# Optimization experiments

Measured on AMD Instinct MI355X. Metric: run time of the kernel, lower is better.

The kernel has to match this reference:

```python
import jax, jax.numpy as jnp
import numpy as np

B = 512        # batch
D = 128        # embedding_dim (n_input)
S = 50         # max_tweets_num (n_sequence)
T = 32         # max_seq_len (n_steps)
HOOPS = 2
NUM_USERS = 20000
NUM_ITEMS = 100000
LATENT = 64
NUM_FRIENDS = 10000
CLIP = 50      # friend_clip
PAD = 50000    # vocab.pad; word table has PAD+1 rows


def setup_inputs() -> dict:
    key = jax.random.key(0)
    ks = jax.random.split(key, 24)
    s = 0.02
    emb_word = (jax.random.normal(ks[0], (PAD + 1, D)) * s).at[PAD].set(0.0)
    emb_item = jax.random.normal(ks[1], (NUM_ITEMS, LATENT)) * s
    emb_user = (jax.random.normal(ks[2], (NUM_FRIENDS + 1, LATENT)) * s).at[NUM_FRIENDS].set(0.0)
    W_mem = jax.random.normal(ks[3], (LATENT, D)) * s
    b_mem = jnp.zeros((D,))
    w_word = jax.random.normal(ks[4], (D,)) * s
    b_word = jnp.zeros(())
    w_sent = jax.random.normal(ks[5], (D,)) * s
    b_sent = jnp.zeros(())
    W_tr = jax.random.normal(ks[6], (D, LATENT)) * s
    b_tr = jnp.zeros((LATENT,))
    W1 = jax.random.normal(ks[7], (LATENT, LATENT // 2)) * s
    b1 = jnp.zeros((LATENT // 2,))
    W2 = jax.random.normal(ks[8], (LATENT // 2, LATENT // 4)) * s
    b2 = jnp.zeros((LATENT // 4,))
    W3 = jax.random.normal(ks[9], (LATENT // 4, 2)) * s
    b3 = jnp.zeros((2,))
    w_aff = jax.random.normal(ks[10], (LATENT,)) * s
    b_aff = jnp.zeros(())
    user_tweet_indices = jax.random.randint(ks[11], (NUM_USERS, S, T), 0, PAD)
    ufi = jax.random.randint(ks[12], (NUM_USERS, CLIP), 0, NUM_FRIENDS)
    # simulate padded friend lists in the trailing slots
    user_friend_indices = ufi.at[:, CLIP - 5:].set(NUM_FRIENDS)
    user_indices = jax.random.randint(ks[13], (B,), 0, NUM_USERS)
    item_indices = jax.random.randint(ks[14], (B,), 0, NUM_ITEMS)
    return {
        'user_indices': user_indices, 'item_indices': item_indices,
        'emb_word': emb_word, 'emb_item': emb_item, 'emb_user': emb_user,
        'W_mem': W_mem, 'b_mem': b_mem, 'w_word': w_word, 'b_word': b_word,
        'w_sent': w_sent, 'b_sent': b_sent, 'W_tr': W_tr, 'b_tr': b_tr,
        'W1': W1, 'b1': b1, 'W2': W2, 'b2': b2, 'W3': W3, 'b3': b3,
        'w_aff': w_aff, 'b_aff': b_aff,
        'user_tweet_indices': user_tweet_indices,
        'user_friend_indices': user_friend_indices,
    }


def reference(user_indices, item_indices, emb_word, emb_item, emb_user,
              W_mem, b_mem, w_word, b_word, w_sent, b_sent, W_tr, b_tr,
              W1, b1, W2, b2, W3, b3, w_aff, b_aff,
              user_tweet_indices, user_friend_indices):
    item_emb = emb_item[item_indices]                       # [B, L]
    mem = item_emb @ W_mem + b_mem                          # [B, D]
    tweets = emb_word[user_tweet_indices[user_indices]]     # [B, S, T, D]
    for _ in range(HOOPS):
        # word-level attention: scores via broadcast mul+sum == einsum
        ww = jax.nn.softmax(jnp.einsum('bstd,bd->bst', tweets, mem), axis=2)
        sentence = jnp.einsum('bst,bstd->bsd', ww, tweets)  # [B, S, D]
        sw = sentence @ w_word + b_word                     # [B, S]
        iw = mem @ w_sent + b_sent                          # [B]
        swf = jax.nn.softmax(jnp.tanh(sw + iw[:, None]), axis=1)
        mem = jnp.einsum('bs,bsd->bd', swf, sentence) + mem
    ept = mem @ W_tr + b_tr                                 # [B, L]
    fidx = user_friend_indices[user_indices]                # [B, C]
    femb = emb_user[fidx]                                   # [B, C, L]
    friend_num = CLIP - (fidx == NUM_FRIENDS).sum(axis=1, keepdims=True).astype(jnp.float32)
    group_idx = jax.nn.sigmoid(
        jnp.einsum('bcl,l->bc', item_emb[:, None, :] * femb, w_aff) + b_aff)[..., None]
    femb = femb * group_idx
    user_emb = femb.sum(axis=1) / friend_num                # [B, L]
    a = jax.nn.sigmoid(item_emb @ W1 + b1)
    a = jax.nn.sigmoid(a @ W2 + b2)
    alpha = jax.nn.sigmoid(a @ W3 + b3)                     # [B, 2]
    vector = alpha[:, 0:1] * ept + alpha[:, 1:2] * user_emb
    rating = jax.nn.sigmoid((vector * item_emb) @ w_aff + b_aff)  # [B]
    return rating, group_idx
```

## Files before the change

### kernel.cpp

```cpp
#include <hip/hip_runtime.h>
#include <hip/hip_fp16.h>

#define NB 512
#define DD 128
#define SS 50
#define TT 32
#define LL 64
#define CLIPN 50
#define NFRIENDS 10000
#define NTHREADS 512
#define NWAVES 8
#define PAD1 50001
#define WELEMS (PAD1 * DD)

typedef unsigned short u16;
typedef unsigned int u32;

__device__ __forceinline__ float bf2f(u32 u) {
    union { u32 i; float f; } c; c.i = u << 16; return c.f;
}
__device__ __forceinline__ u16 f2bf(float f) {
    union { float f; u32 i; } c; c.f = f;
    u32 x = c.i;
    return (u16)((x + 0x7fffu + ((x >> 16) & 1u)) >> 16);
}
__device__ __forceinline__ float sigf(float x) { return 1.f / (1.f + expf(-x)); }

__device__ __forceinline__ void e5m2_dec4(u32 w, float* o) {
    union { u32 u; __half2 h; } lo, hi;
    lo.u = ((w & 0x000000ffu) << 8) | ((w & 0x0000ff00u) << 16);
    hi.u = ((w & 0x00ff0000u) >> 8) | (w & 0xff000000u);
    float2 a = __half22float2(lo.h), b = __half22float2(hi.h);
    o[0] = a.x; o[1] = a.y; o[2] = b.x; o[3] = b.y;
}
__device__ __forceinline__ u32 e5m2_byte(float x) {
    u16 h = __half_as_ushort(__float2half(x));
    u16 r = (u16)(h + 0x7Fu + ((h >> 8) & 1u));
    return (r >> 8) & 0xffu;
}
__device__ __forceinline__ u32 e5m2_enc4(const float* v) {
    return e5m2_byte(v[0]) | (e5m2_byte(v[1]) << 8) |
           (e5m2_byte(v[2]) << 16) | (e5m2_byte(v[3]) << 24);
}

template <bool BF16> struct LD;
template <> struct LD<true> {
    static __device__ __forceinline__ float one(const void* p, long i) {
        return bf2f(((const u16*)p)[i]);
    }
    static __device__ __forceinline__ void st(void* p, long i, float v) {
        ((u16*)p)[i] = f2bf(v);
    }
};
template <> struct LD<false> {
    static __device__ __forceinline__ float one(const void* p, long i) {
        return ((const float*)p)[i];
    }
    static __device__ __forceinline__ void st(void* p, long i, float v) {
        ((float*)p)[i] = v;
    }
};

template <int WM> struct WT;
template <> struct WT<0> {
    static __device__ __forceinline__ void sixteen(const void* p, long i, float* o) {
        const float* s = (const float*)p + i;
        #pragma unroll
        for (int j = 0; j < 4; ++j) {
            float4 v = *(const float4*)(s + 4 * j);
            o[4*j] = v.x; o[4*j+1] = v.y; o[4*j+2] = v.z; o[4*j+3] = v.w;
        }
    }
    static __device__ __forceinline__ void four(const void* p, long i, float* o) {
        float4 v = *(const float4*)((const float*)p + i);
        o[0] = v.x; o[1] = v.y; o[2] = v.z; o[3] = v.w;
    }
};
template <> struct WT<1> {
    static __device__ __forceinline__ void sixteen(const void* p, long i, float* o) {
        const u16* s = (const u16*)p + i;
        #pragma unroll
        for (int j = 0; j < 2; ++j) {
            uint4 v = *(const uint4*)(s + 8 * j);
            float* q = o + 8 * j;
            q[0] = bf2f(v.x & 0xffffu); q[1] = bf2f(v.x >> 16);
            q[2] = bf2f(v.y & 0xffffu); q[3] = bf2f(v.y >> 16);
            q[4] = bf2f(v.z & 0xffffu); q[5] = bf2f(v.z >> 16);
            q[6] = bf2f(v.w & 0xffffu); q[7] = bf2f(v.w >> 16);
        }
    }
    static __device__ __forceinline__ void four(const void* p, long i, float* o) {
        uint2 v = *(const uint2*)((const u16*)p + i);
        o[0] = bf2f(v.x & 0xffffu); o[1] = bf2f(v.x >> 16);
        o[2] = bf2f(v.y & 0xffffu); o[3] = bf2f(v.y >> 16);
    }
};
template <> struct WT<2> {
    static __device__ __forceinline__ void sixteen(const void* p, long i, float* o) {
        uint4 v = *(const uint4*)((const unsigned char*)p + i);
        e5m2_dec4(v.x, o); e5m2_dec4(v.y, o + 4);
        e5m2_dec4(v.z, o + 8); e5m2_dec4(v.w, o + 12);
    }
    static __device__ __forceinline__ void four(const void* p, long i, float* o) {
        e5m2_dec4(*(const u32*)((const unsigned char*)p + i), o);
    }
};

__global__ void sniff_dtype(const void* __restrict__ emb_word, int* __restrict__ flag) {
    const u16* p = (const u16*)emb_word;
    int lane = (int)threadIdx.x;
    int bad = 0;
    #pragma unroll
    for (int j = 0; j < 8; ++j) {
        unsigned e = (p[lane * 8 + j] >> 7) & 0xffu;
        bad += (e >= 127u);
    }
    #pragma unroll
    for (int off = 1; off < 64; off <<= 1) bad += __shfl_xor(bad, off, 64);
    if (lane == 0) flag[0] = (bad <= 16) ? 1 : 0;
}

__global__ void convert_words(const void* __restrict__ src, u32* __restrict__ dst,
                              const int* __restrict__ flag) {
    long idx = (long)blockIdx.x * 256 + threadIdx.x;
    long i = idx * 16;
    if (i >= WELEMS) return;
    float v[16];
    if (flag[0] == 0) {
        const float* s = (const float*)src + i;
        #pragma unroll
        for (int j = 0; j < 4; ++j) {
            float4 q = *(const float4*)(s + 4 * j);
            v[4*j] = q.x; v[4*j+1] = q.y; v[4*j+2] = q.z; v[4*j+3] = q.w;
        }
    } else {
        WT<1>::sixteen(src, i, v);
    }
    uint4 o;
    o.x = e5m2_enc4(v); o.y = e5m2_enc4(v + 4);
    o.z = e5m2_enc4(v + 8); o.w = e5m2_enc4(v + 12);
    *(uint4*)(dst + idx * 4) = o;
}

template <bool BF16, int WM>
__global__ __launch_bounds__(NTHREADS, 4)
void nrs_fused(const int* __restrict__ user_idx,
               const int* __restrict__ item_idx,
               const void* __restrict__ wtab,
               const void* __restrict__ emb_item,
               const void* __restrict__ emb_user,
               const void* __restrict__ W_mem, const void* __restrict__ b_mem,
               const void* __restrict__ w_word, const void* __restrict__ b_word,
               const void* __restrict__ w_sent, const void* __restrict__ b_sent,
               const void* __restrict__ W_tr, const void* __restrict__ b_tr,
               const void* __restrict__ W1, const void* __restrict__ b1,
               const void* __restrict__ W2, const void* __restrict__ b2,
               const void* __restrict__ W3, const void* __restrict__ b3,
               const void* __restrict__ w_aff, const void* __restrict__ b_aff,
               const int* __restrict__ uti, const int* __restrict__ ufi,
               void* __restrict__ out, const int* __restrict__ flag)
{
    if (flag[0] != (BF16 ? 1 : 0)) return;

    __shared__ float s_mem[DD];
    __shared__ float s_item[LL];
    __shared__ float s_sent[SS * DD];
    __shared__ int   s_uti[SS * TT];
    __shared__ float s_sw[SS];
    __shared__ float s_swf[SS];
    __shared__ float s_q[LL];
    __shared__ float s_ept[LL];
    __shared__ float s_uemb[LL];
    __shared__ int   s_fidx[CLIPN];
    __shared__ float s_g[CLIPN];
    __shared__ float s_a1[32];
    __shared__ float s_a2[16];
    __shared__ float s_alpha[2];
    __shared__ float s_fnum;

    const int b = blockIdx.x;
    const int tid = (int)threadIdx.x;
    const int lane = tid & 63;
    const int wave = tid >> 6;

    const int u = user_idx[b];
    const int it = item_idx[b];
    const long utb = (long)u * (SS * TT);

    if (tid < LL) s_item[tid] = LD<BF16>::one(emb_item, (long)it * LL + tid);
    __syncthreads();

    for (int i = tid; i < SS * TT; i += NTHREADS) s_uti[i] = uti[utb + i];
    if (tid < DD) {
        float acc = LD<BF16>::one(b_mem, tid);
        #pragma unroll 8
        for (int l = 0; l < LL; ++l)
            acc += s_item[l] * LD<BF16>::one(W_mem, l * DD + tid);
        s_mem[tid] = acc;
    }
    __syncthreads();

    const float bw = LD<BF16>::one(b_word, 0);
    const float bs = LD<BF16>::one(b_sent, 0);
    const int dq = lane & 31;
    const int th = lane >> 5;
    float ww4[4];
    #pragma unroll
    for (int k = 0; k < 4; ++k) ww4[k] = LD<BF16>::one(w_word, 4 * dq + k);
    const float ws0 = LD<BF16>::one(w_sent, lane);
    const float ws1 = LD<BF16>::one(w_sent, lane + 64);

    for (int hoop = 0; hoop < 2; ++hoop) {
        for (int s = wave; s < SS; s += NWAVES) {
            const int t = lane >> 1, h = lane & 1;
            const int row = s_uti[s * TT + t];
            const long base = (long)row * DD + h * 64;
            float acc = 0.f;
            #pragma unroll
            for (int j = 0; j < 4; ++j) {
                float v16[16];
                WT<WM>::sixteen(wtab, base + 16 * j, v16);
                const float* mp = &s_mem[h * 64 + 16 * j];
                #pragma unroll
                for (int k = 0; k < 16; ++k) acc += v16[k] * mp[k];
            }
            acc += __shfl_xor(acc, 1, 64);

            float mx = acc;
            #pragma unroll
            for (int off = 1; off < 64; off <<= 1) mx = fmaxf(mx, __shfl_xor(mx, off, 64));
            float e = expf(acc - mx);
            float sm = e;
            #pragma unroll
            for (int off = 1; off < 64; off <<= 1) sm += __shfl_xor(sm, off, 64);
            float wwt = 2.f * e / sm;

            float a4[4] = {0.f, 0.f, 0.f, 0.f};
            #pragma unroll 4
            for (int i2 = 0; i2 < 16; ++i2) {
                int t2 = th * 16 + i2;
                float wv = __shfl(wwt, 2 * t2, 64);
                int r2 = s_uti[s * TT + t2];
                float v4[4];
                WT<WM>::four(wtab, (long)r2 * DD + 4 * dq, v4);
                #pragma unroll
                for (int k = 0; k < 4; ++k) a4[k] += wv * v4[k];
            }
            #pragma unroll
            for (int k = 0; k < 4; ++k) a4[k] += __shfl_xor(a4[k], 32, 64);
            if (th == 0)
                *(float4*)&s_sent[s * DD + 4 * dq] =
                    make_float4(a4[0], a4[1], a4[2], a4[3]);

            float p = a4[0] * ww4[0] + a4[1] * ww4[1] + a4[2] * ww4[2] + a4[3] * ww4[3];
            #pragma unroll
            for (int off = 1; off < 64; off <<= 1) p += __shfl_xor(p, off, 64);
            if (lane == 0) s_sw[s] = 0.5f * p + bw;
        }
        __syncthreads();

        if (wave == 0) {
            float p = s_mem[lane] * ws0 + s_mem[lane + 64] * ws1;
            #pragma unroll
            for (int off = 1; off < 64; off <<= 1) p += __shfl_xor(p, off, 64);
            float iw = p + bs;
            float v = (lane < SS) ? tanhf(s_sw[lane] + iw) : -2.f;
            float mx = v;
            #pragma unroll
            for (int off = 1; off < 64; off <<= 1) mx = fmaxf(mx, __shfl_xor(mx, off, 64));
            float e = (lane < SS) ? expf(v - mx) : 0.f;
            float sm = e;
            #pragma unroll
            for (int off = 1; off < 64; off <<= 1) sm += __shfl_xor(sm, off, 64);
            if (lane < SS) s_swf[lane] = e / sm;
        }
        __syncthreads();

        if (tid < DD) {
            float acc = s_mem[tid];
            for (int s2 = 0; s2 < SS; ++s2)
                acc += s_swf[s2] * s_sent[s2 * DD + tid];
            s_mem[tid] = acc;
        }
        __syncthreads();
    }

    if (tid < LL) {
        float acc = LD<BF16>::one(b_tr, tid);
        for (int d = 0; d < DD; ++d)
            acc += s_mem[d] * LD<BF16>::one(W_tr, d * LL + tid);
        s_ept[tid] = acc;
    } else if (tid < 128) {
        int l = tid - 64;
        s_q[l] = s_item[l] * LD<BF16>::one(w_aff, l);
    } else if (tid < 128 + CLIPN) {
        s_fidx[tid - 128] = ufi[(long)u * CLIPN + (tid - 128)];
    } else if (tid >= 192 && tid < 224) {
        int j = tid - 192;
        float acc = LD<BF16>::one(b1, j);
        for (int l = 0; l < LL; ++l)
            acc += s_item[l] * LD<BF16>::one(W1, l * 32 + j);
        s_a1[j] = sigf(acc);
    }
    __syncthreads();

    const float baff = LD<BF16>::one(b_aff, 0);
    if (tid < CLIPN) {
        long fb = (long)s_fidx[tid] * LL;
        float acc = 0.f;
        for (int l = 0; l < LL; ++l) acc += LD<BF16>::one(emb_user, fb + l) * s_q[l];
        float g = sigf(acc + baff);
        s_g[tid] = g;
        LD<BF16>::st(out, NB + (long)b * CLIPN + tid, g);
    } else if (tid >= 64 && tid < 80) {
        int j = tid - 64;
        float acc = LD<BF16>::one(b2, j);
        for (int k = 0; k < 32; ++k) acc += s_a1[k] * LD<BF16>::one(W2, k * 16 + j);
        s_a2[j] = sigf(acc);
    } else if (tid == 80) {
        int cnt = 0;
        for (int c = 0; c < CLIPN; ++c) cnt += (s_fidx[c] == NFRIENDS);
        s_fnum = (float)(CLIPN - cnt);
    }
    __syncthreads();

    if (tid >= 64 && tid < 128) {
        int l = tid - 64;
        float acc = 0.f;
        for (int c = 0; c < CLIPN; ++c)
            acc += s_g[c] * LD<BF16>::one(emb_user, (long)s_fidx[c] * LL + l);
        s_uemb[l] = acc;
    } else if (tid < 2) {
        float acc = LD<BF16>::one(b3, tid);
        for (int k = 0; k < 16; ++k) acc += s_a2[k] * LD<BF16>::one(W3, k * 2 + tid);
        s_alpha[tid] = sigf(acc);
    }
    __syncthreads();

    if (wave == 0) {
        float vec = s_alpha[0] * s_ept[lane] + s_alpha[1] * (s_uemb[lane] / s_fnum);
        float p = vec * s_q[lane];
        #pragma unroll
        for (int off = 1; off < 64; off <<= 1) p += __shfl_xor(p, off, 64);
        if (lane == 0) LD<BF16>::st(out, b, sigf(p + baff));
    }
}

extern "C" void kernel_launch(void* const* d_in, const int* in_sizes, int n_in,
                              void* d_out, int out_size, void* d_ws, size_t ws_size,
                              hipStream_t stream) {
    (void)in_sizes; (void)n_in; (void)out_size;
    int* flag = (int*)d_ws;
    u32* wbuf = (u32*)((char*)d_ws + 64);
    const size_t need = 64 + (size_t)WELEMS;
    const bool ws_ok = ws_size >= need;

    sniff_dtype<<<1, 64, 0, stream>>>(d_in[2], flag);

    #define ARGS(WORDP)                                                        \
        (const int*)d_in[0], (const int*)d_in[1],                              \
        WORDP, d_in[3], d_in[4],                                               \
        d_in[5], d_in[6], d_in[7], d_in[8], d_in[9], d_in[10],                 \
        d_in[11], d_in[12], d_in[13], d_in[14], d_in[15], d_in[16],            \
        d_in[17], d_in[18], d_in[19], d_in[20],                                \
        (const int*)d_in[21], (const int*)d_in[22],                            \
        d_out, (const int*)flag

    if (ws_ok) {
        const long nthr = (WELEMS + 15) / 16;
        convert_words<<<(int)((nthr + 255) / 256), 256, 0, stream>>>(
            d_in[2], wbuf, flag);
        nrs_fused<true, 2><<<NB, NTHREADS, 0, stream>>>(ARGS((const void*)wbuf));
        nrs_fused<false, 2><<<NB, NTHREADS, 0, stream>>>(ARGS((const void*)wbuf));
    } else {
        nrs_fused<true, 1><<<NB, NTHREADS, 0, stream>>>(ARGS(d_in[2]));
        nrs_fused<false, 0><<<NB, NTHREADS, 0, stream>>>(ARGS(d_in[2]));
    }
    #undef ARGS
}
```

Baseline: 304.6 us.

## Use packed fp16 FMA for e5m2 word dots and widen block to 12 waves

New measurement: 328.9 us. +8.0%, slower.

```diff
diff --git a/kernel.cpp b/kernel.cpp
--- a/kernel.cpp
+++ b/kernel.cpp
@@ -8,8 +8,9 @@
 #define LL 64
 #define CLIPN 50
 #define NFRIENDS 10000
-#define NTHREADS 512
-#define NWAVES 8
+#define NTHREADS 768
+#define NWAVES 12
+#define NGROUP 6
 #define PAD1 50001
 #define WELEMS (PAD1 * DD)
 
@@ -26,11 +27,17 @@
 }
 __device__ __forceinline__ float sigf(float x) { return 1.f / (1.f + expf(-x)); }
 
+__device__ __forceinline__ __half2 u2h2(u32 u) {
+    union { u32 u; __half2 h; } c; c.u = u; return c.h;
+}
+__device__ __forceinline__ __half2 e5m2lo(u32 w) {
+    return u2h2(((w & 0x000000ffu) << 8) | ((w & 0x0000ff00u) << 16));
+}
+__device__ __forceinline__ __half2 e5m2hi(u32 w) {
+    return u2h2(((w >> 8) & 0x0000ff00u) | (w & 0xff000000u));
+}
 __device__ __forceinline__ void e5m2_dec4(u32 w, float* o) {
-    union { u32 u; __half2 h; } lo, hi;
-    lo.u = ((w & 0x000000ffu) << 8) | ((w & 0x0000ff00u) << 16);
-    hi.u = ((w & 0x00ff0000u) >> 8) | (w & 0xff000000u);
-    float2 a = __half22float2(lo.h), b = __half22float2(hi.h);
+    float2 a = __half22float2(e5m2lo(w)), b = __half22float2(e5m2hi(w));
     o[0] = a.x; o[1] = a.y; o[2] = b.x; o[3] = b.y;
 }
 __device__ __forceinline__ u32 e5m2_byte(float x) {
@@ -95,16 +102,6 @@
         o[2] = bf2f(v.y & 0xffffu); o[3] = bf2f(v.y >> 16);
     }
 };
-template <> struct WT<2> {
-    static __device__ __forceinline__ void sixteen(const void* p, long i, float* o) {
-        uint4 v = *(const uint4*)((const unsigned char*)p + i);
-        e5m2_dec4(v.x, o); e5m2_dec4(v.y, o + 4);
-        e5m2_dec4(v.z, o + 8); e5m2_dec4(v.w, o + 12);
-    }
-    static __device__ __forceinline__ void four(const void* p, long i, float* o) {
-        e5m2_dec4(*(const u32*)((const unsigned char*)p + i), o);
-    }
-};
 
 __global__ void sniff_dtype(const void* __restrict__ emb_word, int* __restrict__ flag) {
     const u16* p = (const u16*)emb_word;
@@ -143,7 +140,7 @@
 }
 
 template <bool BF16, int WM>
-__global__ __launch_bounds__(NTHREADS, 4)
+__global__ __launch_bounds__(NTHREADS, 6)
 void nrs_fused(const int* __restrict__ user_idx,
                const int* __restrict__ item_idx,
                const void* __restrict__ wtab,
@@ -163,8 +160,10 @@
     if (flag[0] != (BF16 ? 1 : 0)) return;
 
     __shared__ float s_mem[DD];
+    __shared__ __align__(16) u32 s_memh[DD / 2];
     __shared__ float s_item[LL];
     __shared__ float s_sent[SS * DD];
+    __shared__ float s_part[NGROUP * DD];
     __shared__ int   s_uti[SS * TT];
     __shared__ float s_sw[SS];
     __shared__ float s_swf[SS];
@@ -199,6 +198,12 @@
         s_mem[tid] = acc;
     }
     __syncthreads();
+    if (tid < DD / 2) {
+        union { u32 u; __half2 h; } c;
+        c.h = __floats2half2_rn(s_mem[2 * tid], s_mem[2 * tid + 1]);
+        s_memh[tid] = c.u;
+    }
+    __syncthreads();
 
     const float bw = LD<BF16>::one(b_word, 0);
     const float bs = LD<BF16>::one(b_sent, 0);
@@ -209,20 +214,44 @@
     for (int k = 0; k < 4; ++k) ww4[k] = LD<BF16>::one(w_word, 4 * dq + k);
     const float ws0 = LD<BF16>::one(w_sent, lane);
     const float ws1 = LD<BF16>::one(w_sent, lane + 64);
+    const __half2 z2 = __float2half2_rn(0.f);
 
     for (int hoop = 0; hoop < 2; ++hoop) {
         for (int s = wave; s < SS; s += NWAVES) {
             const int t = lane >> 1, h = lane & 1;
             const int row = s_uti[s * TT + t];
-            const long base = (long)row * DD + h * 64;
-            float acc = 0.f;
-            #pragma unroll
-            for (int j = 0; j < 4; ++j) {
-                float v16[16];
-                WT<WM>::sixteen(wtab, base + 16 * j, v16);
-                const float* mp = &s_mem[h * 64 + 16 * j];
+            float acc;
+            if constexpr (WM == 2) {
+                const unsigned char* rp = (const unsigned char*)wtab + (long)row * DD + h * 64;
+                __half2 ah0 = z2, ah1 = z2, ah2 = z2, ah3 = z2;
                 #pragma unroll
-                for (int k = 0; k < 16; ++k) acc += v16[k] * mp[k];
+                for (int j = 0; j < 4; ++j) {
+                    uint4 v = *(const uint4*)(rp + 16 * j);
+                    const u32* mh = &s_memh[h * 32 + 8 * j];
+                    uint4 m0 = *(const uint4*)(mh);
+                    uint4 m1 = *(const uint4*)(mh + 4);
+                    ah0 = __hfma2(e5m2lo(v.x), u2h2(m0.x), ah0);
+                    ah1 = __hfma2(e5m2hi(v.x), u2h2(m0.y), ah1);
+                    ah2 = __hfma2(e5m2lo(v.y), u2h2(m0.z), ah2);
+                    ah3 = __hfma2(e5m2hi(v.y), u2h2(m0.w), ah3);
+                    ah0 = __hfma2(e5m2lo(v.z), u2h2(m1.x), ah0);
+                    ah1 = __hfma2(e5m2hi(v.z), u2h2(m1.y), ah1);
+                    ah2 = __hfma2(e5m2lo(v.w), u2h2(m1.z), ah2);
+                    ah3 = __hfma2(e5m2hi(v.w), u2h2(m1.w), ah3);
+                }
+                __half2 ah = __hadd2(__hadd2(ah0, ah1), __hadd2(ah2, ah3));
+                acc = __low2float(ah) + __high2float(ah);
+            } else {
+                const long base = (long)row * DD + h * 64;
+                acc = 0.f;
+                #pragma unroll
+                for (int j = 0; j < 4; ++j) {
+                    float v16[16];
+                    WT<WM>::sixteen(wtab, base + 16 * j, v16);
+                    const float* mp = &s_mem[h * 64 + 16 * j];
+                    #pragma unroll
+                    for (int k = 0; k < 16; ++k) acc += v16[k] * mp[k];
+                }
             }
             acc += __shfl_xor(acc, 1, 64);
 
@@ -235,24 +264,42 @@
             for (int off = 1; off < 64; off <<= 1) sm += __shfl_xor(sm, off, 64);
             float wwt = 2.f * e / sm;
 
-            float a4[4] = {0.f, 0.f, 0.f, 0.f};
-            #pragma unroll 4
-            for (int i2 = 0; i2 < 16; ++i2) {
-                int t2 = th * 16 + i2;
-                float wv = __shfl(wwt, 2 * t2, 64);
-                int r2 = s_uti[s * TT + t2];
-                float v4[4];
-                WT<WM>::four(wtab, (long)r2 * DD + 4 * dq, v4);
-                #pragma unroll
-                for (int k = 0; k < 4; ++k) a4[k] += wv * v4[k];
+            float a0, a1, a2, a3;
+            if constexpr (WM == 2) {
+                __half2 p01 = z2, p23 = z2;
+                #pragma unroll 4
+                for (int i2 = 0; i2 < 16; ++i2) {
+                    int t2 = th * 16 + i2;
+                    float wv = __shfl(wwt, 2 * t2, 64);
+                    int r2 = s_uti[s * TT + t2];
+                    u32 w = *(const u32*)((const unsigned char*)wtab + (long)r2 * DD + 4 * dq);
+                    __half2 wvh = __float2half2_rn(wv);
+                    p01 = __hfma2(wvh, e5m2lo(w), p01);
+                    p23 = __hfma2(wvh, e5m2hi(w), p23);
+                }
+                a0 = __low2float(p01); a1 = __high2float(p01);
+                a2 = __low2float(p23); a3 = __high2float(p23);
+            } else {
+                a0 = a1 = a2 = a3 = 0.f;
+                #pragma unroll 4
+                for (int i2 = 0; i2 < 16; ++i2) {
+                    int t2 = th * 16 + i2;
+                    float wv = __shfl(wwt, 2 * t2, 64);
+                    int r2 = s_uti[s * TT + t2];
+                    float v4[4];
+                    WT<WM>::four(wtab, (long)r2 * DD + 4 * dq, v4);
+                    a0 += wv * v4[0]; a1 += wv * v4[1];
+                    a2 += wv * v4[2]; a3 += wv * v4[3];
+                }
             }
-            #pragma unroll
-            for (int k = 0; k < 4; ++k) a4[k] += __shfl_xor(a4[k], 32, 64);
+            a0 += __shfl_xor(a0, 32, 64);
+            a1 += __shfl_xor(a1, 32, 64);
+            a2 += __shfl_xor(a2, 32, 64);
+            a3 += __shfl_xor(a3, 32, 64);
             if (th == 0)
-                *(float4*)&s_sent[s * DD + 4 * dq] =
-                    make_float4(a4[0], a4[1], a4[2], a4[3]);
-
-            float p = a4[0] * ww4[0] + a4[1] * ww4[1] + a4[2] * ww4[2] + a4[3] * ww4[3];
+                *(float4*)&s_sent[s * DD + 4 * dq] = make_float4(a0, a1, a2, a3);
+
+            float p = a0 * ww4[0] + a1 * ww4[1] + a2 * ww4[2] + a3 * ww4[3];
             #pragma unroll
             for (int off = 1; off < 64; off <<= 1) p += __shfl_xor(p, off, 64);
             if (lane == 0) s_sw[s] = 0.5f * p + bw;
@@ -276,11 +323,26 @@
         }
         __syncthreads();
 
-        if (tid < DD) {
-            float acc = s_mem[tid];
-            for (int s2 = 0; s2 < SS; ++s2)
-                acc += s_swf[s2] * s_sent[s2 * DD + tid];
-            s_mem[tid] = acc;
+        {
+            int g = tid >> 7;
+            int d = tid & (DD - 1);
+            float acc = 0.f;
+            for (int s2 = g; s2 < SS; s2 += NGROUP)
+                acc += s_swf[s2] * s_sent[s2 * DD + d];
+            s_part[g * DD + d] = acc;
+        }
+        __syncthreads();
+        if (tid < DD / 2) {
+            float a0 = s_mem[2 * tid], a1 = s_mem[2 * tid + 1];
+            #pragma unroll
+            for (int g = 0; g < NGROUP; ++g) {
+                a0 += s_part[g * DD + 2 * tid];
+                a1 += s_part[g * DD + 2 * tid + 1];
+            }
+            s_mem[2 * tid] = a0; s_mem[2 * tid + 1] = a1;
+            union { u32 u; __half2 h; } c;
+            c.h = __floats2half2_rn(a0, a1);
+            s_memh[tid] = c.u;
         }
         __syncthreads();
     }
```
